# Kernel tuning notes

Hardware: AMD Instinct MI355X
Metric: run time of the kernel (lower is better)

## Reference

```python
import jax, jax.numpy as jnp
import numpy as np

N = 8192
TAU = 0.5
B = 4096


def _factorize(n, tau):
    # Precompute LU factorization of the tridiagonal implicit-Laplace matrix,
    # mirroring the torch __init__ exactly.
    b = np.full(n - 1, -tau, dtype=np.float32)   # upper diagonal
    a = np.full(n, 1.0 + 2.0 * tau, dtype=np.float32)  # main diagonal
    c = np.full(n - 1, -tau, dtype=np.float32)   # lower diagonal
    a[0] = 1.0 + tau
    a[-1] = 1.0 + tau
    for i in range(n - 1):
        c[i] = c[i] / a[i]
        a[i + 1] = a[i + 1] - c[i] * b[i]
    return a, b, c


def setup_inputs() -> dict:
    key = jax.random.key(0)
    a, b, c = _factorize(N, TAU)
    x = jax.random.normal(key, (B, N), dtype=jnp.float32)
    return {
        "x": x,
        "a": jnp.asarray(a),
        "b": jnp.asarray(b),
        "c": jnp.asarray(c),
    }


def reference(x, a, b, c):
    # Thomas algorithm with precomputed LU factors.
    # Forward substitution:  y[0] = x[0];  y[i] = x[i] - y[i-1] * c[i-1]
    # Back substitution:     z[N-1] = y[N-1] / a[N-1];
    #                        z[i]   = (y[i] - z[i+1] * b[i]) / a[i]
    xt = x.T  # [N, B] so the scan runs over the grid axis
    c_pad = jnp.concatenate([jnp.zeros((1,), x.dtype), c])  # c_pad[0]=0 -> y[0]=x[0]

    def fwd_step(y_prev, inp):
        xi, ci = inp
        yi = xi - y_prev * ci
        return yi, yi

    _, y = jax.lax.scan(fwd_step, jnp.zeros_like(xt[0]), (xt, c_pad))

    b_pad = jnp.concatenate([b, jnp.zeros((1,), x.dtype)])  # b_pad[N-1]=0

    def bwd_step(z_next, inp):
        yi, bi, ai = inp
        zi = (yi - z_next * bi) / ai
        return zi, zi

    _, z = jax.lax.scan(bwd_step, jnp.zeros_like(y[0]), (y, b_pad, a), reverse=True)
    return z.T  # [B, N]
```

## Files before the change

kernel.cpp:

```cpp
#include <hip/hip_runtime.h>


#define NN    8192
#define BB    4096
#define CHUNK 64
#define HALO  16
#define WIN   (CHUNK + HALO)

typedef float yvec_t __attribute__((ext_vector_type(WIN)));

__device__ __forceinline__ float fast_rcp(float v) {
    float r = __builtin_amdgcn_rcpf(v);
    return r * (2.0f - v * r);
}

template<bool FIRST, bool EDGE>
__device__ __forceinline__ void solve_window(
    const float* __restrict__ xrow,
    const float* __restrict__ a,
    const float* __restrict__ b,
    const float* __restrict__ c,
    float* __restrict__ orow,
    int s)
{
    const float* xs = xrow + s;
    const float* as = a + s;
    const float* bs = b + s;
    const float* cs = c + s;

    float y = 0.0f;

    if (!FIRST) {
        const float* xw = xrow + (s - HALO);
        const float* cw = c + (s - HALO);
        #pragma unroll
        for (int k = 0; k < HALO; k += 4) {
            float4 xv = *(const float4*)(xw + k);
            y = xv.x - cw[k - 1] * y;
            y = xv.y - cw[k]     * y;
            y = xv.z - cw[k + 1] * y;
            y = xv.w - cw[k + 2] * y;
        }
    }

    yvec_t ybuf;
    #pragma unroll
    for (int k = 0; k < (EDGE ? CHUNK : WIN); k += 4) {
        float4 xv = *(const float4*)(xs + k);
        float c0 = (FIRST && k == 0) ? 0.0f : cs[k - 1];
        y = xv.x - c0        * y;  ybuf[k]     = y;
        y = xv.y - cs[k]     * y;  ybuf[k + 1] = y;
        y = xv.z - cs[k + 1] * y;  ybuf[k + 2] = y;
        y = xv.w - cs[k + 2] * y;  ybuf[k + 3] = y;
    }

    float z = 0.0f;
    if (!EDGE) {
        #pragma unroll
        for (int k = WIN - 1; k >= CHUNK; --k) {
            z = (ybuf[k] - bs[k] * z) * fast_rcp(as[k]);
        }
        #pragma unroll
        for (int k = CHUNK - 1; k >= 0; --k) {
            z = (ybuf[k] - bs[k] * z) * fast_rcp(as[k]);
            ybuf[k] = z;
        }
    } else {
        z = ybuf[CHUNK - 1] * fast_rcp(as[CHUNK - 1]);
        ybuf[CHUNK - 1] = z;
        #pragma unroll
        for (int k = CHUNK - 2; k >= 0; --k) {
            z = (ybuf[k] - bs[k] * z) * fast_rcp(as[k]);
            ybuf[k] = z;
        }
    }

    #pragma unroll
    for (int k = 0; k < CHUNK; k += 4) {
        float4 zv;
        zv.x = ybuf[k];
        zv.y = ybuf[k + 1];
        zv.z = ybuf[k + 2];
        zv.w = ybuf[k + 3];
        *(float4*)(orow + s + k) = zv;
    }
}

__global__ __launch_bounds__(256, 4) void TriDiagonalLaplaceSolver_kernel(
    const float* __restrict__ x,
    const float* __restrict__ a,
    const float* __restrict__ b,
    const float* __restrict__ c,
    float* __restrict__ out)
{
    const int chunk = blockIdx.x;
    const int row   = blockIdx.y * 256 + threadIdx.x;
    const int s     = chunk * CHUNK;

    const float* xrow = x   + (size_t)row * NN;
    float*       orow = out + (size_t)row * NN;

    if (chunk == 0) {
        solve_window<true, false>(xrow, a, b, c, orow, 0);
    } else if (chunk == (NN / CHUNK) - 1) {
        solve_window<false, true>(xrow, a, b, c, orow, s);
    } else {
        solve_window<false, false>(xrow, a, b, c, orow, s);
    }
}

extern "C" void kernel_launch(void* const* d_in, const int* in_sizes, int n_in,
                              void* d_out, int out_size, void* d_ws, size_t ws_size,
                              hipStream_t stream) {
    const float* x = (const float*)d_in[0];
    const float* a = (const float*)d_in[1];
    const float* b = (const float*)d_in[2];
    const float* c = (const float*)d_in[3];
    float* out = (float*)d_out;

    dim3 grid(NN / CHUNK, BB / 256);
    dim3 block(256);
    TriDiagonalLaplaceSolver_kernel<<<grid, block, 0, stream>>>(x, a, b, c, out);
}
```

Measured before the change: 309.0 us.

## Stage row tiles in LDS for coalesced loads and stores, precompute reciprocals

Each block now stages a 32-row by 4-chunk tile of x, with halos, into swizzled shared memory using coalesced float4 loads. Threads then run the windowed Thomas solve out of LDS, and results go back through LDS for coalesced row-contiguous stores. Before, each thread read and wrote its own row with a stride of NN, so accesses were uncoalesced. The coefficients c, b and 1/a are loaded once per block into LDS, which also shares the halo reads between adjacent chunks. The costs are extra LDS traffic, barriers, and lower occupancy from the large shared tile.

```diff
diff --git a/kernel.cpp b/kernel.cpp
--- a/kernel.cpp
+++ b/kernel.cpp
@@ -3,9 +3,14 @@
 
 #define NN    8192
 #define BB    4096
+#define ROWS  32
+#define CCOL  4
 #define CHUNK 64
 #define HALO  16
-#define WIN   (CHUNK + HALO)
+#define TILE_F   (CCOL*CHUNK + 2*HALO)
+#define TILE_F4  (TILE_F/4)
+#define WIN      (CHUNK + HALO)
+#define NTHR     (ROWS*CCOL)
 
 typedef float yvec_t __attribute__((ext_vector_type(WIN)));
 
@@ -14,98 +19,105 @@
     return r * (2.0f - v * r);
 }
 
-template<bool FIRST, bool EDGE>
-__device__ __forceinline__ void solve_window(
-    const float* __restrict__ xrow,
-    const float* __restrict__ a,
-    const float* __restrict__ b,
-    const float* __restrict__ c,
-    float* __restrict__ orow,
-    int s)
-{
-    const float* xs = xrow + s;
-    const float* as = a + s;
-    const float* bs = b + s;
-    const float* cs = c + s;
-
-    float y = 0.0f;
-
-    if (!FIRST) {
-        const float* xw = xrow + (s - HALO);
-        const float* cw = c + (s - HALO);
-        #pragma unroll
-        for (int k = 0; k < HALO; k += 4) {
-            float4 xv = *(const float4*)(xw + k);
-            y = xv.x - cw[k - 1] * y;
-            y = xv.y - cw[k]     * y;
-            y = xv.z - cw[k + 1] * y;
-            y = xv.w - cw[k + 2] * y;
-        }
-    }
-
-    yvec_t ybuf;
-    #pragma unroll
-    for (int k = 0; k < (EDGE ? CHUNK : WIN); k += 4) {
-        float4 xv = *(const float4*)(xs + k);
-        float c0 = (FIRST && k == 0) ? 0.0f : cs[k - 1];
-        y = xv.x - c0        * y;  ybuf[k]     = y;
-        y = xv.y - cs[k]     * y;  ybuf[k + 1] = y;
-        y = xv.z - cs[k + 1] * y;  ybuf[k + 2] = y;
-        y = xv.w - cs[k + 2] * y;  ybuf[k + 3] = y;
-    }
-
-    float z = 0.0f;
-    if (!EDGE) {
-        #pragma unroll
-        for (int k = WIN - 1; k >= CHUNK; --k) {
-            z = (ybuf[k] - bs[k] * z) * fast_rcp(as[k]);
-        }
-        #pragma unroll
-        for (int k = CHUNK - 1; k >= 0; --k) {
-            z = (ybuf[k] - bs[k] * z) * fast_rcp(as[k]);
-            ybuf[k] = z;
-        }
-    } else {
-        z = ybuf[CHUNK - 1] * fast_rcp(as[CHUNK - 1]);
-        ybuf[CHUNK - 1] = z;
-        #pragma unroll
-        for (int k = CHUNK - 2; k >= 0; --k) {
-            z = (ybuf[k] - bs[k] * z) * fast_rcp(as[k]);
-            ybuf[k] = z;
-        }
-    }
-
-    #pragma unroll
-    for (int k = 0; k < CHUNK; k += 4) {
-        float4 zv;
-        zv.x = ybuf[k];
-        zv.y = ybuf[k + 1];
-        zv.z = ybuf[k + 2];
-        zv.w = ybuf[k + 3];
-        *(float4*)(orow + s + k) = zv;
-    }
-}
-
-__global__ __launch_bounds__(256, 4) void TriDiagonalLaplaceSolver_kernel(
+__global__ __launch_bounds__(NTHR, 2) void TriDiagonalLaplaceSolver_kernel(
     const float* __restrict__ x,
     const float* __restrict__ a,
     const float* __restrict__ b,
     const float* __restrict__ c,
     float* __restrict__ out)
 {
-    const int chunk = blockIdx.x;
-    const int row   = blockIdx.y * 256 + threadIdx.x;
-    const int s     = chunk * CHUNK;
+    __shared__ float4 tile[ROWS * TILE_F4];
+    __shared__ __align__(16) float scm[TILE_F];
+    __shared__ __align__(16) float srb[TILE_F];
+    __shared__ __align__(16) float sra[TILE_F];
 
-    const float* xrow = x   + (size_t)row * NN;
-    float*       orow = out + (size_t)row * NN;
+    const int t  = threadIdx.x;
+    const int g  = blockIdx.x;
+    const int r0 = blockIdx.y * ROWS;
+    const int S0 = g * (CCOL*CHUNK) - HALO;
 
-    if (chunk == 0) {
-        solve_window<true, false>(xrow, a, b, c, orow, 0);
-    } else if (chunk == (NN / CHUNK) - 1) {
-        solve_window<false, true>(xrow, a, b, c, orow, s);
-    } else {
-        solve_window<false, false>(xrow, a, b, c, orow, s);
+    for (int j = t; j < TILE_F; j += NTHR) {
+        const int G = S0 + j;
+        scm[j] = (G >= 1 && G <= NN-1) ? c[G-1]         : 0.0f;
+        srb[j] = (G >= 0 && G <= NN-2) ? b[G]           : 0.0f;
+        sra[j] = (G >= 0 && G <= NN-1) ? fast_rcp(a[G]) : 0.0f;
+    }
+
+    const float4* __restrict__ x4 = (const float4*)x;
+    const int S4 = (S0 >> 2);
+    #pragma unroll
+    for (int it = 0; it < (ROWS*TILE_F4)/NTHR; ++it) {
+        const int i  = it*NTHR + t;
+        const int rr = i / TILE_F4;
+        const int c4 = i - rr*TILE_F4;
+        const int G4 = S4 + c4;
+        float4 v = make_float4(0.0f, 0.0f, 0.0f, 0.0f);
+        if (G4 >= 0 && G4 < NN/4)
+            v = x4[(r0 + rr) * (NN/4) + G4];
+        tile[rr*TILE_F4 + (c4 ^ (rr & 7))] = v;
+    }
+    __syncthreads();
+
+    const int row = t & (ROWS-1);
+    const int cc  = t >> 5;
+    const int sw  = row & 7;
+    const int tb  = row * TILE_F4;
+    const int cb  = cc * CHUNK;
+    const int cb4 = cb >> 2;
+
+    float y = 0.0f;
+    yvec_t ybuf;
+    #pragma unroll
+    for (int q = 0; q < (HALO + WIN)/4; ++q) {
+        const float4 xv = tile[tb + ((cb4 + q) ^ sw)];
+        const float4 cm = *(const float4*)&scm[cb + 4*q];
+        const float y0 = xv.x - cm.x * y;
+        const float y1 = xv.y - cm.y * y0;
+        const float y2 = xv.z - cm.z * y1;
+        const float y3 = xv.w - cm.w * y2;
+        y = y3;
+        if (q >= HALO/4) {
+            const int k = 4*q - HALO;
+            ybuf[k] = y0; ybuf[k+1] = y1; ybuf[k+2] = y2; ybuf[k+3] = y3;
+        }
+    }
+
+    float z = 0.0f;
+    #pragma unroll
+    for (int q = WIN/4 - 1; q >= 0; --q) {
+        const int colf = cb + HALO + 4*q;
+        const float4 bv = *(const float4*)&srb[colf];
+        const float4 rv = *(const float4*)&sra[colf];
+        const int k = 4*q;
+        const float z3 = (ybuf[k+3] - bv.w * z ) * rv.w;
+        const float z2 = (ybuf[k+2] - bv.z * z3) * rv.z;
+        const float z1 = (ybuf[k+1] - bv.y * z2) * rv.y;
+        const float z0 = (ybuf[k+0] - bv.x * z1) * rv.x;
+        z = z0;
+        if (q < CHUNK/4) {
+            ybuf[k] = z0; ybuf[k+1] = z1; ybuf[k+2] = z2; ybuf[k+3] = z3;
+        }
+    }
+
+    __syncthreads();
+
+    #pragma unroll
+    for (int q = 0; q < CHUNK/4; ++q) {
+        float4 zv;
+        zv.x = ybuf[4*q];   zv.y = ybuf[4*q+1];
+        zv.z = ybuf[4*q+2]; zv.w = ybuf[4*q+3];
+        tile[tb + ((cb4 + HALO/4 + q) ^ sw)] = zv;
+    }
+    __syncthreads();
+
+    float4* __restrict__ o4 = (float4*)out;
+    #pragma unroll
+    for (int it = 0; it < (ROWS*CCOL*CHUNK/4)/NTHR; ++it) {
+        const int i   = it*NTHR + t;
+        const int rr  = i >> 6;
+        const int c4o = i & 63;
+        const float4 v = tile[rr*TILE_F4 + ((c4o + HALO/4) ^ (rr & 7))];
+        o4[(r0 + rr) * (NN/4) + g*(CCOL*CHUNK/4) + c4o] = v;
     }
 }
 
@@ -118,7 +130,7 @@
     const float* c = (const float*)d_in[3];
     float* out = (float*)d_out;
 
-    dim3 grid(NN / CHUNK, BB / 256);
-    dim3 block(256);
+    dim3 grid(NN / (CCOL*CHUNK), BB / ROWS);
+    dim3 block(NTHR);
     TriDiagonalLaplaceSolver_kernel<<<grid, block, 0, stream>>>(x, a, b, c, out);
 }
```

Result: slower. 328.6 us (+6.3%).
